# Kernel tuning notes

Hardware: AMD Instinct MI355X
Metric: run time of the kernel (lower is better)

## Reference

```python
import jax, jax.numpy as jnp
import numpy as np

N, E = 50000, 800000
IN_DIM, HID, OUT, HEADS = 128, 128, 64, 4
C1 = HID // HEADS  # 32 per-head channels in gat1
NEG_SLOPE = 0.2


def _gat_conv(x, src, dst, W, a_src, a_dst, b, heads, ch):
    """PyG GATConv (inference): gather -> edge attention -> segment softmax -> scatter."""
    n = x.shape[0]
    h = (x @ W).reshape(n, heads, ch)                      # [N,H,C]
    alpha_src = jnp.einsum('nhc,hc->nh', h, a_src)         # [N,H]
    alpha_dst = jnp.einsum('nhc,hc->nh', h, a_dst)         # [N,H]
    e = jax.nn.leaky_relu(alpha_src[src] + alpha_dst[dst], NEG_SLOPE)  # [E,H]
    m = jax.ops.segment_max(e, dst, num_segments=n)        # per-target max (stable softmax)
    e = jnp.exp(e - m[dst])
    denom = jax.ops.segment_sum(e, dst, num_segments=n)
    alpha = e / (denom[dst] + 1e-16)                       # [E,H]
    out = jax.ops.segment_sum(h[src] * alpha[:, :, None], dst, num_segments=n)  # [N,H,C]
    return out.reshape(n, heads * ch) + b


def setup_inputs() -> dict:
    key = jax.random.key(0)
    ks = jax.random.split(key, 16)
    x = jax.random.normal(ks[0], (N, IN_DIM), dtype=jnp.float32)
    edge_index = jax.random.randint(ks[1], (2, E), 0, N, dtype=jnp.int64)
    s = lambda fan_in: 1.0 / np.sqrt(fan_in)
    return {
        'x': x,
        'edge_index': edge_index,
        'W1': jax.random.normal(ks[2], (IN_DIM, HEADS * C1), jnp.float32) * s(IN_DIM),
        'a_src1': jax.random.normal(ks[3], (HEADS, C1), jnp.float32) * s(C1),
        'a_dst1': jax.random.normal(ks[4], (HEADS, C1), jnp.float32) * s(C1),
        'b1': jnp.zeros((HID,), jnp.float32),
        'W2': jax.random.normal(ks[5], (HID, OUT), jnp.float32) * s(HID),
        'a_src2': jax.random.normal(ks[6], (1, OUT), jnp.float32) * s(OUT),
        'a_dst2': jax.random.normal(ks[7], (1, OUT), jnp.float32) * s(OUT),
        'b2': jnp.zeros((OUT,), jnp.float32),
        'pw1': jax.random.normal(ks[8], (OUT, OUT), jnp.float32) * s(OUT),
        'pb1': jnp.zeros((OUT,), jnp.float32),
        'pw2': jax.random.normal(ks[9], (OUT, OUT), jnp.float32) * s(OUT),
        'pb2': jnp.zeros((OUT,), jnp.float32),
    }


def reference(x, edge_index, W1, a_src1, a_dst1, b1, W2, a_src2, a_dst2, b2, pw1, pb1, pw2, pb2):
    n = x.shape[0]
    # PyG GATConv add_self_loops=True
    loops = jnp.arange(n, dtype=edge_index.dtype)
    src = jnp.concatenate([edge_index[0], loops])
    dst = jnp.concatenate([edge_index[1], loops])
    h = jax.nn.elu(_gat_conv(x, src, dst, W1, a_src1, a_dst1, b1, HEADS, C1))
    h = jax.nn.elu(_gat_conv(h, src, dst, W2, a_src2, a_dst2, b2, 1, OUT))
    # origin_proj: Linear -> ReLU -> Linear
    h = jax.nn.relu(h @ pw1 + pb1)
    return h @ pw2 + pb2
```

## Files before the change

### kernel.cpp

```cpp
#include <hip/hip_runtime.h>
#include <math.h>

#define N_NODES 50000
#define N_EDGES 800000
#define ET (N_EDGES + N_NODES)
#define IN_DIM 128
#define HID 128
#define OUT_DIM 64
#define BW 64
#define NBUCK ((N_NODES + BW - 1) / BW)
#define NBLK 256
#define EPB 3328
#define NT64 ((N_NODES + 63) / 64)

typedef __attribute__((ext_vector_type(8))) short bf16x8;
typedef __attribute__((ext_vector_type(4))) float f32x4;

__device__ __forceinline__ float lrelu(float x){ return x >= 0.f ? x : 0.2f * x; }
__device__ __forceinline__ float eluf(float x){ return x > 0.f ? x : expm1f(x); }
__device__ __forceinline__ unsigned f2bf(float f){
    unsigned u = __float_as_uint(f);
    return (u + 0x7fffu + ((u >> 16) & 1u)) >> 16;
}
__device__ __forceinline__ float bflo(unsigned u){ return __uint_as_float(u << 16); }
__device__ __forceinline__ float bfhi(unsigned u){ return __uint_as_float(u & 0xffff0000u); }

__global__ __launch_bounds__(256) void k_count(const int* __restrict__ dst, int* __restrict__ C)
{
    __shared__ int cnt[NBUCK];
    const int tid = threadIdx.x, blk = blockIdx.x;
    for (int i = tid; i < NBUCK; i += 256) cnt[i] = 0;
    __syncthreads();
    #pragma unroll
    for (int j = 0; j < EPB / 256; j++) {
        const int e = blk * EPB + j * 256 + tid;
        if (e < ET) {
            const int d = (e < N_EDGES) ? dst[e] : (e - N_EDGES);
            atomicAdd(&cnt[d >> 6], 1);
        }
    }
    __syncthreads();
    for (int b = tid; b < NBUCK; b += 256) C[b * NBLK + blk] = cnt[b];
}

__global__ __launch_bounds__(256) void k_bsumA(const int* __restrict__ C, int* __restrict__ bsum2)
{
    __shared__ int red[4];
    int v = C[blockIdx.x * NBLK + threadIdx.x];
    #pragma unroll
    for (int off = 32; off > 0; off >>= 1) v += __shfl_down(v, off);
    if ((threadIdx.x & 63) == 0) red[threadIdx.x >> 6] = v;
    __syncthreads();
    if (threadIdx.x == 0) bsum2[blockIdx.x] = red[0] + red[1] + red[2] + red[3];
}

__global__ __launch_bounds__(1024) void k_bscanB(const int* __restrict__ bsum2, int* __restrict__ boff2)
{
    __shared__ int part[1024];
    const int t = threadIdx.x;
    int v = (t < NBUCK) ? bsum2[t] : 0;
    part[t] = v;
    __syncthreads();
    #pragma unroll
    for (int d = 1; d < 1024; d <<= 1) {
        int add = (t >= d) ? part[t - d] : 0;
        __syncthreads();
        part[t] += add;
        __syncthreads();
    }
    if (t < NBUCK) boff2[t] = part[t] - v;
    if (t == 0) boff2[NBUCK] = ET;
}

__global__ __launch_bounds__(256) void k_cscanC(const int* __restrict__ C,
                                                const int* __restrict__ boff2,
                                                int* __restrict__ Cs)
{
    __shared__ int part[256];
    const int t = threadIdx.x, b = blockIdx.x;
    int v = C[b * NBLK + t];
    part[t] = v;
    __syncthreads();
    #pragma unroll
    for (int d = 1; d < 256; d <<= 1) {
        int add = (t >= d) ? part[t - d] : 0;
        __syncthreads();
        part[t] += add;
        __syncthreads();
    }
    Cs[b * NBLK + t] = boff2[b] + part[t] - v;
}

__global__ __launch_bounds__(256, 2) void k_gemm1_part2(
    const float* __restrict__ x, const float* __restrict__ W1,
    const float* __restrict__ a_s, const float* __restrict__ a_d,
    unsigned* __restrict__ h1b, float* __restrict__ as1, float* __restrict__ ad1,
    const int* __restrict__ src, const int* __restrict__ dst,
    const int* __restrict__ Cs, uint2* __restrict__ part)
{
    __shared__ unsigned smem[128 * 68 + 64 * 68];
    const int tid = threadIdx.x;

    if (blockIdx.x < NT64) {
        unsigned* sWt = smem;
        unsigned* sxb = smem + 128 * 68;
        const int wave = tid >> 6;
        const int lane = tid & 63;
        const int ll   = lane & 15;
        const int quad = lane >> 4;
        const int n0 = blockIdx.x * 64;

        for (int idx = tid; idx < 8192; idx += 256) {
            const int n = idx & 127, kp = idx >> 7;
            const float w0 = W1[(2 * kp) * 128 + n];
            const float w1 = W1[(2 * kp + 1) * 128 + n];
            sWt[n * 68 + kp] = f2bf(w0) | (f2bf(w1) << 16);
        }
        for (int idx = tid; idx < 4096; idx += 256) {
            const int node = idx >> 6, kp = idx & 63;
            const int n = n0 + node;
            unsigned pk = 0;
            if (n < N_NODES) {
                const float x0 = x[n * 128 + 2 * kp];
                const float x1 = x[n * 128 + 2 * kp + 1];
                pk = f2bf(x0) | (f2bf(x1) << 16);
            }
            sxb[node * 68 + kp] = pk;
        }
        __syncthreads();

        f32x4 acc[8];
        #pragma unroll
        for (int t = 0; t < 8; t++) acc[t] = (f32x4){0.f, 0.f, 0.f, 0.f};

        #pragma unroll
        for (int kk = 0; kk < 4; kk++) {
            const int kpo = 16 * kk + 4 * quad;
            const bf16x8 a = *(const bf16x8*)&sxb[(16 * wave + ll) * 68 + kpo];
            #pragma unroll
            for (int t = 0; t < 8; t++) {
                const bf16x8 b = *(const bf16x8*)&sWt[(16 * t + ll) * 68 + kpo];
                acc[t] = __builtin_amdgcn_mfma_f32_16x16x32_bf16(a, b, acc[t], 0, 0, 0);
            }
        }

        float as_v[8], ad_v[8];
        #pragma unroll
        for (int t = 0; t < 8; t++) { as_v[t] = a_s[16 * t + ll]; ad_v[t] = a_d[16 * t + ll]; }
        unsigned short* h1u = (unsigned short*)h1b;
        #pragma unroll
        for (int r = 0; r < 4; r++) {
            const int n = n0 + 16 * wave + 4 * quad + r;
            float ps0 = acc[0][r] * as_v[0] + acc[1][r] * as_v[1];
            float ps1 = acc[2][r] * as_v[2] + acc[3][r] * as_v[3];
            float ps2 = acc[4][r] * as_v[4] + acc[5][r] * as_v[5];
            float ps3 = acc[6][r] * as_v[6] + acc[7][r] * as_v[7];
            float pd0 = acc[0][r] * ad_v[0] + acc[1][r] * ad_v[1];
            float pd1 = acc[2][r] * ad_v[2] + acc[3][r] * ad_v[3];
            float pd2 = acc[4][r] * ad_v[4] + acc[5][r] * ad_v[5];
            float pd3 = acc[6][r] * ad_v[6] + acc[7][r] * ad_v[7];
            #pragma unroll
            for (int off = 1; off < 16; off <<= 1) {
                ps0 += __shfl_xor(ps0, off); ps1 += __shfl_xor(ps1, off);
                ps2 += __shfl_xor(ps2, off); ps3 += __shfl_xor(ps3, off);
                pd0 += __shfl_xor(pd0, off); pd1 += __shfl_xor(pd1, off);
                pd2 += __shfl_xor(pd2, off); pd3 += __shfl_xor(pd3, off);
            }
            if (n < N_NODES) {
                #pragma unroll
                for (int t = 0; t < 8; t++)
                    h1u[n * 128 + 16 * t + ll] = (unsigned short)f2bf(acc[t][r]);
                if (ll == 0) {
                    as1[n * 4 + 0] = ps0; as1[n * 4 + 1] = ps1;
                    as1[n * 4 + 2] = ps2; as1[n * 4 + 3] = ps3;
                    ad1[n * 4 + 0] = pd0; ad1[n * 4 + 1] = pd1;
                    ad1[n * 4 + 2] = pd2; ad1[n * 4 + 3] = pd3;
                }
            }
        }
    } else {
        const int blk = blockIdx.x - NT64;
        int* base = (int*)smem;
        int* cnt  = (int*)smem + NBUCK;
        for (int b = tid; b < NBUCK; b += 256) { base[b] = Cs[b * NBLK + blk]; cnt[b] = 0; }
        __syncthreads();
        #pragma unroll
        for (int j = 0; j < EPB / 256; j++) {
            const int e = blk * EPB + j * 256 + tid;
            if (e < ET) {
                int s, d;
                if (e < N_EDGES) { s = src[e]; d = dst[e]; } else { s = d = e - N_EDGES; }
                const int b = d >> 6;
                const int r = atomicAdd(&cnt[b], 1);
                part[base[b] + r] = make_uint2((unsigned)d, (unsigned)s);
            }
        }
    }
}

__global__ __launch_bounds__(256) void k_scat2(const int* __restrict__ boff2,
                                               const uint2* __restrict__ part,
                                               int* __restrict__ rowptr,
                                               int* __restrict__ csr_src)
{
    __shared__ int cnt64[BW];
    __shared__ int nbase[BW];
    const int b = blockIdx.x, tid = threadIdx.x;
    const int n0 = b * BW;
    const int lo = boff2[b], hi = boff2[b + 1];
    if (tid < BW) cnt64[tid] = 0;
    __syncthreads();
    for (int i = lo + tid; i < hi; i += 256) {
        atomicAdd(&cnt64[part[i].x & (BW - 1)], 1);
    }
    __syncthreads();
    if (tid < BW) {
        int v = cnt64[tid];
        int incl = v;
        #pragma unroll
        for (int off = 1; off < 64; off <<= 1) {
            int t2 = __shfl_up(incl, off);
            if (tid >= off) incl += t2;
        }
        const int excl = incl - v;
        nbase[tid] = excl;
        const int n = n0 + tid;
        if (n < N_NODES) rowptr[n] = lo + excl;
        cnt64[tid] = 0;
    }
    if (b == 0 && tid == 0) rowptr[N_NODES] = ET;
    __syncthreads();
    for (int i = lo + tid; i < hi; i += 256) {
        const uint2 p = part[i];
        const int dn = (int)p.x & (BW - 1);
        const int r = atomicAdd(&cnt64[dn], 1);
        csr_src[lo + nbase[dn] + r] = (int)p.y;
    }
}

__global__ __launch_bounds__(256) void k_aggr1(
    const int* __restrict__ rowptr, const int* __restrict__ csr_src,
    const float* __restrict__ as1, const float* __restrict__ ad1,
    const uint4* __restrict__ h1u4, const float* __restrict__ b1,
    unsigned* __restrict__ hEb)
{
    const int d  = blockIdx.x * 16 + (threadIdx.x >> 4);
    const int c8 = threadIdx.x & 15;
    const int hd = c8 >> 2;
    const int r0 = rowptr[d], r1 = rowptr[d + 1];
    const float adv = ad1[d * 4 + hd];
    float den = 0.f;
    float acc[8];
    #pragma unroll
    for (int m = 0; m < 8; m++) acc[m] = 0.f;
    int i = r0;
    for (; i + 4 <= r1; i += 4) {
        const int s0 = csr_src[i],     s1 = csr_src[i + 1];
        const int s2 = csr_src[i + 2], s3 = csr_src[i + 3];
        const float e0 = as1[s0 * 4 + hd], e1 = as1[s1 * 4 + hd];
        const float e2 = as1[s2 * 4 + hd], e3 = as1[s3 * 4 + hd];
        const uint4 u0 = h1u4[s0 * 16 + c8];
        const uint4 u1 = h1u4[s1 * 16 + c8];
        const uint4 u2 = h1u4[s2 * 16 + c8];
        const uint4 u3 = h1u4[s3 * 16 + c8];
        const float w0 = expf(lrelu(e0 + adv));
        const float w1 = expf(lrelu(e1 + adv));
        const float w2 = expf(lrelu(e2 + adv));
        const float w3 = expf(lrelu(e3 + adv));
        den += (w0 + w1) + (w2 + w3);
        acc[0] = fmaf(bflo(u0.x), w0, acc[0]); acc[1] = fmaf(bfhi(u0.x), w0, acc[1]);
        acc[2] = fmaf(bflo(u0.y), w0, acc[2]); acc[3] = fmaf(bfhi(u0.y), w0, acc[3]);
        acc[4] = fmaf(bflo(u0.z), w0, acc[4]); acc[5] = fmaf(bfhi(u0.z), w0, acc[5]);
        acc[6] = fmaf(bflo(u0.w), w0, acc[6]); acc[7] = fmaf(bfhi(u0.w), w0, acc[7]);
        acc[0] = fmaf(bflo(u1.x), w1, acc[0]); acc[1] = fmaf(bfhi(u1.x), w1, acc[1]);
        acc[2] = fmaf(bflo(u1.y), w1, acc[2]); acc[3] = fmaf(bfhi(u1.y), w1, acc[3]);
        acc[4] = fmaf(bflo(u1.z), w1, acc[4]); acc[5] = fmaf(bfhi(u1.z), w1, acc[5]);
        acc[6] = fmaf(bflo(u1.w), w1, acc[6]); acc[7] = fmaf(bfhi(u1.w), w1, acc[7]);
        acc[0] = fmaf(bflo(u2.x), w2, acc[0]); acc[1] = fmaf(bfhi(u2.x), w2, acc[1]);
        acc[2] = fmaf(bflo(u2.y), w2, acc[2]); acc[3] = fmaf(bfhi(u2.y), w2, acc[3]);
        acc[4] = fmaf(bflo(u2.z), w2, acc[4]); acc[5] = fmaf(bfhi(u2.z), w2, acc[5]);
        acc[6] = fmaf(bflo(u2.w), w2, acc[6]); acc[7] = fmaf(bfhi(u2.w), w2, acc[7]);
        acc[0] = fmaf(bflo(u3.x), w3, acc[0]); acc[1] = fmaf(bfhi(u3.x), w3, acc[1]);
        acc[2] = fmaf(bflo(u3.y), w3, acc[2]); acc[3] = fmaf(bfhi(u3.y), w3, acc[3]);
        acc[4] = fmaf(bflo(u3.z), w3, acc[4]); acc[5] = fmaf(bfhi(u3.z), w3, acc[5]);
        acc[6] = fmaf(bflo(u3.w), w3, acc[6]); acc[7] = fmaf(bfhi(u3.w), w3, acc[7]);
    }
    for (; i < r1; ++i) {
        const int s = csr_src[i];
        const float w = expf(lrelu(as1[s * 4 + hd] + adv));
        const uint4 u = h1u4[s * 16 + c8];
        den += w;
        acc[0] = fmaf(bflo(u.x), w, acc[0]); acc[1] = fmaf(bfhi(u.x), w, acc[1]);
        acc[2] = fmaf(bflo(u.y), w, acc[2]); acc[3] = fmaf(bfhi(u.y), w, acc[3]);
        acc[4] = fmaf(bflo(u.z), w, acc[4]); acc[5] = fmaf(bfhi(u.z), w, acc[5]);
        acc[6] = fmaf(bflo(u.w), w, acc[6]); acc[7] = fmaf(bfhi(u.w), w, acc[7]);
    }
    const float inv = 1.f / (den + 1e-16f);
    const float4 bA = ((const float4*)b1)[2 * c8];
    const float4 bB = ((const float4*)b1)[2 * c8 + 1];
    const float v0 = eluf(acc[0] * inv + bA.x);
    const float v1 = eluf(acc[1] * inv + bA.y);
    const float v2 = eluf(acc[2] * inv + bA.z);
    const float v3 = eluf(acc[3] * inv + bA.w);
    const float v4 = eluf(acc[4] * inv + bB.x);
    const float v5 = eluf(acc[5] * inv + bB.y);
    const float v6 = eluf(acc[6] * inv + bB.z);
    const float v7 = eluf(acc[7] * inv + bB.w);
    uint4 o;
    o.x = f2bf(v0) | (f2bf(v1) << 16);
    o.y = f2bf(v2) | (f2bf(v3) << 16);
    o.z = f2bf(v4) | (f2bf(v5) << 16);
    o.w = f2bf(v6) | (f2bf(v7) << 16);
    ((uint4*)hEb)[d * 16 + c8] = o;
}

__global__ __launch_bounds__(256, 4) void k_layer2(
    const unsigned* __restrict__ hEb,
    const float* __restrict__ W2, const float* __restrict__ a_s2, const float* __restrict__ a_d2,
    unsigned* __restrict__ h2b, float* __restrict__ as2, float* __restrict__ ad2)
{
    __shared__ unsigned sWt[64 * 68];
    __shared__ unsigned sxb[64 * 68];
    const int tid = threadIdx.x;
    const int wave = tid >> 6;
    const int lane = tid & 63;
    const int ll   = lane & 15;
    const int quad = lane >> 4;
    const int n0 = blockIdx.x * 64;

    for (int idx = tid; idx < 4096; idx += 256) {
        const int n = idx & 63, kp = idx >> 6;
        const float w0 = W2[(2 * kp) * 64 + n];
        const float w1 = W2[(2 * kp + 1) * 64 + n];
        sWt[n * 68 + kp] = f2bf(w0) | (f2bf(w1) << 16);
    }
    const uint4* hE4 = (const uint4*)hEb;
    for (int idx = tid; idx < 1024; idx += 256) {
        const int node = idx >> 4, q = idx & 15;
        const int n = n0 + node;
        uint4 pk = make_uint4(0, 0, 0, 0);
        if (n < N_NODES) pk = hE4[n * 16 + q];
        unsigned* dstp = &sxb[node * 68 + 4 * q];
        dstp[0] = pk.x; dstp[1] = pk.y; dstp[2] = pk.z; dstp[3] = pk.w;
    }
    __syncthreads();

    f32x4 acc[4];
    #pragma unroll
    for (int t = 0; t < 4; t++) acc[t] = (f32x4){0.f, 0.f, 0.f, 0.f};

    #pragma unroll
    for (int kk = 0; kk < 4; kk++) {
        const int kpo = 16 * kk + 4 * quad;
        const bf16x8 a = *(const bf16x8*)&sxb[(16 * wave + ll) * 68 + kpo];
        #pragma unroll
        for (int t = 0; t < 4; t++) {
            const bf16x8 b = *(const bf16x8*)&sWt[(16 * t + ll) * 68 + kpo];
            acc[t] = __builtin_amdgcn_mfma_f32_16x16x32_bf16(a, b, acc[t], 0, 0, 0);
        }
    }

    float as_v[4], ad_v[4];
    #pragma unroll
    for (int t = 0; t < 4; t++) { as_v[t] = a_s2[16 * t + ll]; ad_v[t] = a_d2[16 * t + ll]; }
    unsigned short* h2u = (unsigned short*)h2b;
    #pragma unroll
    for (int r = 0; r < 4; r++) {
        const int n = n0 + 16 * wave + 4 * quad + r;
        float ps = acc[0][r] * as_v[0] + acc[1][r] * as_v[1]
                 + acc[2][r] * as_v[2] + acc[3][r] * as_v[3];
        float pd = acc[0][r] * ad_v[0] + acc[1][r] * ad_v[1]
                 + acc[2][r] * ad_v[2] + acc[3][r] * ad_v[3];
        #pragma unroll
        for (int off = 1; off < 16; off <<= 1) {
            ps += __shfl_xor(ps, off);
            pd += __shfl_xor(pd, off);
        }
        if (n < N_NODES) {
            #pragma unroll
            for (int t = 0; t < 4; t++)
                h2u[n * 64 + 16 * t + ll] = (unsigned short)f2bf(acc[t][r]);
            if (ll == 0) { as2[n] = ps; ad2[n] = pd; }
        }
    }
}

__global__ __launch_bounds__(512, 4) void k_tail(
    const int* __restrict__ rowptr, const int* __restrict__ csr_src,
    const float* __restrict__ as2, const float* __restrict__ ad2,
    const uint4* __restrict__ h2u4, const float* __restrict__ b2,
    const float* __restrict__ pw1, const float* __restrict__ pb1,
    const float* __restrict__ pw2, const float* __restrict__ pb2,
    float* __restrict__ out)
{
    __shared__ float s1[64 * 64];
    __shared__ float s2[64 * 64];
    __shared__ float so[64][68];
    __shared__ float sp[64][68];
    const int tid = threadIdx.x;
    const int n0 = blockIdx.x * 64;

    for (int i = tid; i < 1024; i += 512) {
        ((float4*)s1)[i] = ((const float4*)pw1)[i];
        ((float4*)s2)[i] = ((const float4*)pw2)[i];
    }

    {
        const int dl = tid >> 3;
        const int c8 = tid & 7;
        const int d = n0 + dl;
        float acc[8];
        #pragma unroll
        for (int m = 0; m < 8; m++) acc[m] = 0.f;
        float v0 = 0.f, v1 = 0.f, v2 = 0.f, v3 = 0.f;
        float v4 = 0.f, v5 = 0.f, v6 = 0.f, v7 = 0.f;
        if (d < N_NODES) {
            const int r0 = rowptr[d], r1 = rowptr[d + 1];
            const float adv = ad2[d];
            float den = 0.f;
            int i = r0;
            for (; i + 4 <= r1; i += 4) {
                const int s0 = csr_src[i],     s1_ = csr_src[i + 1];
                const int s2_ = csr_src[i + 2], s3_ = csr_src[i + 3];
                const float e0 = as2[s0], e1 = as2[s1_], e2 = as2[s2_], e3 = as2[s3_];
                const uint4 u0 = h2u4[s0  * 8 + c8];
                const uint4 u1 = h2u4[s1_ * 8 + c8];
                const uint4 u2 = h2u4[s2_ * 8 + c8];
                const uint4 u3 = h2u4[s3_ * 8 + c8];
                const float w0 = expf(lrelu(e0 + adv));
                const float w1 = expf(lrelu(e1 + adv));
                const float w2 = expf(lrelu(e2 + adv));
                const float w3 = expf(lrelu(e3 + adv));
                den += (w0 + w1) + (w2 + w3);
                acc[0] = fmaf(bflo(u0.x), w0, acc[0]); acc[1] = fmaf(bfhi(u0.x), w0, acc[1]);
                acc[2] = fmaf(bflo(u0.y), w0, acc[2]); acc[3] = fmaf(bfhi(u0.y), w0, acc[3]);
                acc[4] = fmaf(bflo(u0.z), w0, acc[4]); acc[5] = fmaf(bfhi(u0.z), w0, acc[5]);
                acc[6] = fmaf(bflo(u0.w), w0, acc[6]); acc[7] = fmaf(bfhi(u0.w), w0, acc[7]);
                acc[0] = fmaf(bflo(u1.x), w1, acc[0]); acc[1] = fmaf(bfhi(u1.x), w1, acc[1]);
                acc[2] = fmaf(bflo(u1.y), w1, acc[2]); acc[3] = fmaf(bfhi(u1.y), w1, acc[3]);
                acc[4] = fmaf(bflo(u1.z), w1, acc[4]); acc[5] = fmaf(bfhi(u1.z), w1, acc[5]);
                acc[6] = fmaf(bflo(u1.w), w1, acc[6]); acc[7] = fmaf(bfhi(u1.w), w1, acc[7]);
                acc[0] = fmaf(bflo(u2.x), w2, acc[0]); acc[1] = fmaf(bfhi(u2.x), w2, acc[1]);
                acc[2] = fmaf(bflo(u2.y), w2, acc[2]); acc[3] = fmaf(bfhi(u2.y), w2, acc[3]);
                acc[4] = fmaf(bflo(u2.z), w2, acc[4]); acc[5] = fmaf(bfhi(u2.z), w2, acc[5]);
                acc[6] = fmaf(bflo(u2.w), w2, acc[6]); acc[7] = fmaf(bfhi(u2.w), w2, acc[7]);
                acc[0] = fmaf(bflo(u3.x), w3, acc[0]); acc[1] = fmaf(bfhi(u3.x), w3, acc[1]);
                acc[2] = fmaf(bflo(u3.y), w3, acc[2]); acc[3] = fmaf(bfhi(u3.y), w3, acc[3]);
                acc[4] = fmaf(bflo(u3.z), w3, acc[4]); acc[5] = fmaf(bfhi(u3.z), w3, acc[5]);
                acc[6] = fmaf(bflo(u3.w), w3, acc[6]); acc[7] = fmaf(bfhi(u3.w), w3, acc[7]);
            }
            for (; i < r1; ++i) {
                const int s = csr_src[i];
                const float w = expf(lrelu(as2[s] + adv));
                const uint4 u = h2u4[s * 8 + c8];
                den += w;
                acc[0] = fmaf(bflo(u.x), w, acc[0]); acc[1] = fmaf(bfhi(u.x), w, acc[1]);
                acc[2] = fmaf(bflo(u.y), w, acc[2]); acc[3] = fmaf(bfhi(u.y), w, acc[3]);
                acc[4] = fmaf(bflo(u.z), w, acc[4]); acc[5] = fmaf(bfhi(u.z), w, acc[5]);
                acc[6] = fmaf(bflo(u.w), w, acc[6]); acc[7] = fmaf(bfhi(u.w), w, acc[7]);
            }
            const float inv = 1.f / (den + 1e-16f);
            const float4 bA = ((const float4*)b2)[2 * c8];
            const float4 bB = ((const float4*)b2)[2 * c8 + 1];
            v0 = eluf(acc[0] * inv + bA.x);
            v1 = eluf(acc[1] * inv + bA.y);
            v2 = eluf(acc[2] * inv + bA.z);
            v3 = eluf(acc[3] * inv + bA.w);
            v4 = eluf(acc[4] * inv + bB.x);
            v5 = eluf(acc[5] * inv + bB.y);
            v6 = eluf(acc[6] * inv + bB.z);
            v7 = eluf(acc[7] * inv + bB.w);
        }
        *(float4*)&so[dl][8 * c8]     = make_float4(v0, v1, v2, v3);
        *(float4*)&so[dl][8 * c8 + 4] = make_float4(v4, v5, v6, v7);
    }
    __syncthreads();

    const int cg = tid & 15;
    const int ng = tid >> 4;
    const float4 pb1_4 = ((const float4*)pb1)[cg];
    const float4 pb2_4 = ((const float4*)pb2)[cg];
    float4 p[2];
    #pragma unroll
    for (int m = 0; m < 2; m++) p[m] = pb1_4;
    #pragma unroll 8
    for (int k = 0; k < 64; k++) {
        const float4 w = *(const float4*)&s1[k * 64 + 4 * cg];
        #pragma unroll
        for (int m = 0; m < 2; m++) {
            const float xv = so[2 * ng + m][k];
            p[m].x = fmaf(xv, w.x, p[m].x);
            p[m].y = fmaf(xv, w.y, p[m].y);
            p[m].z = fmaf(xv, w.z, p[m].z);
            p[m].w = fmaf(xv, w.w, p[m].w);
        }
    }
    #pragma unroll
    for (int m = 0; m < 2; m++) {
        p[m].x = fmaxf(p[m].x, 0.f); p[m].y = fmaxf(p[m].y, 0.f);
        p[m].z = fmaxf(p[m].z, 0.f); p[m].w = fmaxf(p[m].w, 0.f);
        *(float4*)&sp[2 * ng + m][4 * cg] = p[m];
    }
    __syncthreads();
    float4 o[2];
    #pragma unroll
    for (int m = 0; m < 2; m++) o[m] = pb2_4;
    #pragma unroll 8
    for (int k = 0; k < 64; k++) {
        const float4 w = *(const float4*)&s2[k * 64 + 4 * cg];
        #pragma unroll
        for (int m = 0; m < 2; m++) {
            const float xv = sp[2 * ng + m][k];
            o[m].x = fmaf(xv, w.x, o[m].x);
            o[m].y = fmaf(xv, w.y, o[m].y);
            o[m].z = fmaf(xv, w.z, o[m].z);
            o[m].w = fmaf(xv, w.w, o[m].w);
        }
    }
    #pragma unroll
    for (int m = 0; m < 2; m++) {
        const int n = n0 + 2 * ng + m;
        if (n < N_NODES) ((float4*)out)[n * 16 + cg] = o[m];
    }
}

extern "C" void kernel_launch(void* const* d_in, const int* in_sizes, int n_in,
                              void* d_out, int out_size, void* d_ws, size_t ws_size,
                              hipStream_t stream)
{
    const float* x      = (const float*)d_in[0];
    const int*   ei     = (const int*)d_in[1];
    const int*   src    = ei;
    const int*   dst    = ei + N_EDGES;
    const float* W1     = (const float*)d_in[2];
    const float* a_src1 = (const float*)d_in[3];
    const float* a_dst1 = (const float*)d_in[4];
    const float* b1     = (const float*)d_in[5];
    const float* W2     = (const float*)d_in[6];
    const float* a_src2 = (const float*)d_in[7];
    const float* a_dst2 = (const float*)d_in[8];
    const float* b2     = (const float*)d_in[9];
    const float* pw1    = (const float*)d_in[10];
    const float* pb1    = (const float*)d_in[11];
    const float* pw2    = (const float*)d_in[12];
    const float* pb2    = (const float*)d_in[13];

    uint2* part  = (uint2*)d_ws;
    int* ibase   = (int*)(part + ET);
    int* rowptr  = ibase;
    int* C       = rowptr + 50001;
    int* Cs      = C + 200192;
    int* bsum2   = Cs + 200192;
    int* boff2   = bsum2 + 782;
    int* csr_src = boff2 + 785;
    unsigned* h1b = (unsigned*)(csr_src + 850000);
    unsigned* h2b = h1b + 3200000;
    float* fws   = (float*)(h2b + 1600000);
    float* as1   = fws;
    float* ad1   = as1 + 200000;
    unsigned* hEb = (unsigned*)(ad1 + 200000);
    float* as2   = (float*)(hEb + 3200000);
    float* ad2   = as2 + 50000;

    k_count<<<NBLK, 256, 0, stream>>>(dst, C);
    k_bsumA<<<NBUCK, 256, 0, stream>>>(C, bsum2);
    k_bscanB<<<1, 1024, 0, stream>>>(bsum2, boff2);
    k_cscanC<<<NBUCK, 256, 0, stream>>>(C, boff2, Cs);

    k_gemm1_part2<<<NT64 + NBLK, 256, 0, stream>>>(x, W1, a_src1, a_dst1,
                                                   h1b, as1, ad1,
                                                   src, dst, Cs, part);
    k_scat2<<<NBUCK, 256, 0, stream>>>(boff2, part, rowptr, csr_src);

    k_aggr1<<<N_NODES / 16, 256, 0, stream>>>(rowptr, csr_src, as1, ad1,
                                              (const uint4*)h1b, b1, hEb);

    k_layer2<<<NT64, 256, 0, stream>>>(hEb, W2, a_src2, a_dst2, h2b, as2, ad2);

    k_tail<<<NT64, 512, 0, stream>>>(rowptr, csr_src, as2, ad2,
                                     (const uint4*)h2b, b2,
                                     pw1, pb1, pw2, pb2, (float*)d_out);
}
```

Measured before the change: 224.1 us.

## Fuse layer-1 aggregation with layer-2 GEMM and fold bucket sums into count

The layer-1 attention aggregation now writes its ELU'd bf16 rows straight into shared memory, and the same block runs the layer-2 MFMA projection. This removes the hEb round trip through global memory and one kernel launch. Per-bucket totals are now accumulated with atomics inside k_count after a memset, which replaces the separate k_bsumA kernel. k_tail reuses one shared buffer for both MLP stages to raise occupancy, at the cost of an extra barrier. Only 128 of 512 threads do the MFMA work, and 8 waves per block wait at the barrier behind the slowest gather.

```diff
diff --git a/kernel.cpp b/kernel.cpp
--- a/kernel.cpp
+++ b/kernel.cpp
@@ -12,6 +12,7 @@
 #define NBLK 256
 #define EPB 3328
 #define NT64 ((N_NODES + 63) / 64)
+#define NT32 ((N_NODES + 31) / 32)
 
 typedef __attribute__((ext_vector_type(8))) short bf16x8;
 typedef __attribute__((ext_vector_type(4))) float f32x4;
@@ -25,7 +26,9 @@
 __device__ __forceinline__ float bflo(unsigned u){ return __uint_as_float(u << 16); }
 __device__ __forceinline__ float bfhi(unsigned u){ return __uint_as_float(u & 0xffff0000u); }
 
-__global__ __launch_bounds__(256) void k_count(const int* __restrict__ dst, int* __restrict__ C)
+__global__ __launch_bounds__(256) void k_count(const int* __restrict__ dst,
+                                               int* __restrict__ C,
+                                               int* __restrict__ bsum2)
 {
     __shared__ int cnt[NBUCK];
     const int tid = threadIdx.x, blk = blockIdx.x;
@@ -40,18 +43,11 @@
         }
     }
     __syncthreads();
-    for (int b = tid; b < NBUCK; b += 256) C[b * NBLK + blk] = cnt[b];
-}
-
-__global__ __launch_bounds__(256) void k_bsumA(const int* __restrict__ C, int* __restrict__ bsum2)
-{
-    __shared__ int red[4];
-    int v = C[blockIdx.x * NBLK + threadIdx.x];
-    #pragma unroll
-    for (int off = 32; off > 0; off >>= 1) v += __shfl_down(v, off);
-    if ((threadIdx.x & 63) == 0) red[threadIdx.x >> 6] = v;
-    __syncthreads();
-    if (threadIdx.x == 0) bsum2[blockIdx.x] = red[0] + red[1] + red[2] + red[3];
+    for (int b = tid; b < NBUCK; b += 256) {
+        const int v = cnt[b];
+        C[b * NBLK + blk] = v;
+        if (v) atomicAdd(&bsum2[b], v);
+    }
 }
 
 __global__ __launch_bounds__(1024) void k_bscanB(const int* __restrict__ bsum2, int* __restrict__ boff2)
@@ -238,154 +234,149 @@
     }
 }
 
-__global__ __launch_bounds__(256) void k_aggr1(
+__global__ __launch_bounds__(512, 8) void k_aggr1_l2(
     const int* __restrict__ rowptr, const int* __restrict__ csr_src,
     const float* __restrict__ as1, const float* __restrict__ ad1,
     const uint4* __restrict__ h1u4, const float* __restrict__ b1,
-    unsigned* __restrict__ hEb)
-{
-    const int d  = blockIdx.x * 16 + (threadIdx.x >> 4);
-    const int c8 = threadIdx.x & 15;
-    const int hd = c8 >> 2;
-    const int r0 = rowptr[d], r1 = rowptr[d + 1];
-    const float adv = ad1[d * 4 + hd];
-    float den = 0.f;
-    float acc[8];
-    #pragma unroll
-    for (int m = 0; m < 8; m++) acc[m] = 0.f;
-    int i = r0;
-    for (; i + 4 <= r1; i += 4) {
-        const int s0 = csr_src[i],     s1 = csr_src[i + 1];
-        const int s2 = csr_src[i + 2], s3 = csr_src[i + 3];
-        const float e0 = as1[s0 * 4 + hd], e1 = as1[s1 * 4 + hd];
-        const float e2 = as1[s2 * 4 + hd], e3 = as1[s3 * 4 + hd];
-        const uint4 u0 = h1u4[s0 * 16 + c8];
-        const uint4 u1 = h1u4[s1 * 16 + c8];
-        const uint4 u2 = h1u4[s2 * 16 + c8];
-        const uint4 u3 = h1u4[s3 * 16 + c8];
-        const float w0 = expf(lrelu(e0 + adv));
-        const float w1 = expf(lrelu(e1 + adv));
-        const float w2 = expf(lrelu(e2 + adv));
-        const float w3 = expf(lrelu(e3 + adv));
-        den += (w0 + w1) + (w2 + w3);
-        acc[0] = fmaf(bflo(u0.x), w0, acc[0]); acc[1] = fmaf(bfhi(u0.x), w0, acc[1]);
-        acc[2] = fmaf(bflo(u0.y), w0, acc[2]); acc[3] = fmaf(bfhi(u0.y), w0, acc[3]);
-        acc[4] = fmaf(bflo(u0.z), w0, acc[4]); acc[5] = fmaf(bfhi(u0.z), w0, acc[5]);
-        acc[6] = fmaf(bflo(u0.w), w0, acc[6]); acc[7] = fmaf(bfhi(u0.w), w0, acc[7]);
-        acc[0] = fmaf(bflo(u1.x), w1, acc[0]); acc[1] = fmaf(bfhi(u1.x), w1, acc[1]);
-        acc[2] = fmaf(bflo(u1.y), w1, acc[2]); acc[3] = fmaf(bfhi(u1.y), w1, acc[3]);
-        acc[4] = fmaf(bflo(u1.z), w1, acc[4]); acc[5] = fmaf(bfhi(u1.z), w1, acc[5]);
-        acc[6] = fmaf(bflo(u1.w), w1, acc[6]); acc[7] = fmaf(bfhi(u1.w), w1, acc[7]);
-        acc[0] = fmaf(bflo(u2.x), w2, acc[0]); acc[1] = fmaf(bfhi(u2.x), w2, acc[1]);
-        acc[2] = fmaf(bflo(u2.y), w2, acc[2]); acc[3] = fmaf(bfhi(u2.y), w2, acc[3]);
-        acc[4] = fmaf(bflo(u2.z), w2, acc[4]); acc[5] = fmaf(bfhi(u2.z), w2, acc[5]);
-        acc[6] = fmaf(bflo(u2.w), w2, acc[6]); acc[7] = fmaf(bfhi(u2.w), w2, acc[7]);
-        acc[0] = fmaf(bflo(u3.x), w3, acc[0]); acc[1] = fmaf(bfhi(u3.x), w3, acc[1]);
-        acc[2] = fmaf(bflo(u3.y), w3, acc[2]); acc[3] = fmaf(bfhi(u3.y), w3, acc[3]);
-        acc[4] = fmaf(bflo(u3.z), w3, acc[4]); acc[5] = fmaf(bfhi(u3.z), w3, acc[5]);
-        acc[6] = fmaf(bflo(u3.w), w3, acc[6]); acc[7] = fmaf(bfhi(u3.w), w3, acc[7]);
-    }
-    for (; i < r1; ++i) {
-        const int s = csr_src[i];
-        const float w = expf(lrelu(as1[s * 4 + hd] + adv));
-        const uint4 u = h1u4[s * 16 + c8];
-        den += w;
-        acc[0] = fmaf(bflo(u.x), w, acc[0]); acc[1] = fmaf(bfhi(u.x), w, acc[1]);
-        acc[2] = fmaf(bflo(u.y), w, acc[2]); acc[3] = fmaf(bfhi(u.y), w, acc[3]);
-        acc[4] = fmaf(bflo(u.z), w, acc[4]); acc[5] = fmaf(bfhi(u.z), w, acc[5]);
-        acc[6] = fmaf(bflo(u.w), w, acc[6]); acc[7] = fmaf(bfhi(u.w), w, acc[7]);
-    }
-    const float inv = 1.f / (den + 1e-16f);
-    const float4 bA = ((const float4*)b1)[2 * c8];
-    const float4 bB = ((const float4*)b1)[2 * c8 + 1];
-    const float v0 = eluf(acc[0] * inv + bA.x);
-    const float v1 = eluf(acc[1] * inv + bA.y);
-    const float v2 = eluf(acc[2] * inv + bA.z);
-    const float v3 = eluf(acc[3] * inv + bA.w);
-    const float v4 = eluf(acc[4] * inv + bB.x);
-    const float v5 = eluf(acc[5] * inv + bB.y);
-    const float v6 = eluf(acc[6] * inv + bB.z);
-    const float v7 = eluf(acc[7] * inv + bB.w);
-    uint4 o;
-    o.x = f2bf(v0) | (f2bf(v1) << 16);
-    o.y = f2bf(v2) | (f2bf(v3) << 16);
-    o.z = f2bf(v4) | (f2bf(v5) << 16);
-    o.w = f2bf(v6) | (f2bf(v7) << 16);
-    ((uint4*)hEb)[d * 16 + c8] = o;
-}
-
-__global__ __launch_bounds__(256, 4) void k_layer2(
-    const unsigned* __restrict__ hEb,
     const float* __restrict__ W2, const float* __restrict__ a_s2, const float* __restrict__ a_d2,
     unsigned* __restrict__ h2b, float* __restrict__ as2, float* __restrict__ ad2)
 {
     __shared__ unsigned sWt[64 * 68];
-    __shared__ unsigned sxb[64 * 68];
+    __shared__ unsigned sxb[32 * 68];
     const int tid = threadIdx.x;
-    const int wave = tid >> 6;
-    const int lane = tid & 63;
-    const int ll   = lane & 15;
-    const int quad = lane >> 4;
-    const int n0 = blockIdx.x * 64;
-
-    for (int idx = tid; idx < 4096; idx += 256) {
+    const int n0 = blockIdx.x * 32;
+
+    for (int idx = tid; idx < 4096; idx += 512) {
         const int n = idx & 63, kp = idx >> 6;
         const float w0 = W2[(2 * kp) * 64 + n];
         const float w1 = W2[(2 * kp + 1) * 64 + n];
         sWt[n * 68 + kp] = f2bf(w0) | (f2bf(w1) << 16);
     }
-    const uint4* hE4 = (const uint4*)hEb;
-    for (int idx = tid; idx < 1024; idx += 256) {
-        const int node = idx >> 4, q = idx & 15;
-        const int n = n0 + node;
-        uint4 pk = make_uint4(0, 0, 0, 0);
-        if (n < N_NODES) pk = hE4[n * 16 + q];
-        unsigned* dstp = &sxb[node * 68 + 4 * q];
-        dstp[0] = pk.x; dstp[1] = pk.y; dstp[2] = pk.z; dstp[3] = pk.w;
-    }
-    __syncthreads();
-
-    f32x4 acc[4];
-    #pragma unroll
-    for (int t = 0; t < 4; t++) acc[t] = (f32x4){0.f, 0.f, 0.f, 0.f};
-
-    #pragma unroll
-    for (int kk = 0; kk < 4; kk++) {
-        const int kpo = 16 * kk + 4 * quad;
-        const bf16x8 a = *(const bf16x8*)&sxb[(16 * wave + ll) * 68 + kpo];
-        #pragma unroll
-        for (int t = 0; t < 4; t++) {
-            const bf16x8 b = *(const bf16x8*)&sWt[(16 * t + ll) * 68 + kpo];
-            acc[t] = __builtin_amdgcn_mfma_f32_16x16x32_bf16(a, b, acc[t], 0, 0, 0);
-        }
-    }
-
-    float as_v[4], ad_v[4];
-    #pragma unroll
-    for (int t = 0; t < 4; t++) { as_v[t] = a_s2[16 * t + ll]; ad_v[t] = a_d2[16 * t + ll]; }
-    unsigned short* h2u = (unsigned short*)h2b;
-    #pragma unroll
-    for (int r = 0; r < 4; r++) {
-        const int n = n0 + 16 * wave + 4 * quad + r;
-        float ps = acc[0][r] * as_v[0] + acc[1][r] * as_v[1]
-                 + acc[2][r] * as_v[2] + acc[3][r] * as_v[3];
-        float pd = acc[0][r] * ad_v[0] + acc[1][r] * ad_v[1]
-                 + acc[2][r] * ad_v[2] + acc[3][r] * ad_v[3];
-        #pragma unroll
-        for (int off = 1; off < 16; off <<= 1) {
-            ps += __shfl_xor(ps, off);
-            pd += __shfl_xor(pd, off);
-        }
-        if (n < N_NODES) {
+
+    {
+        const int dl = tid >> 4;
+        const int c8 = tid & 15;
+        const int hd = c8 >> 2;
+        const int d = n0 + dl;
+        uint4 o = make_uint4(0, 0, 0, 0);
+        if (d < N_NODES) {
+            const int r0 = rowptr[d], r1 = rowptr[d + 1];
+            const float adv = ad1[d * 4 + hd];
+            float den = 0.f;
+            float acc[8];
             #pragma unroll
-            for (int t = 0; t < 4; t++)
-                h2u[n * 64 + 16 * t + ll] = (unsigned short)f2bf(acc[t][r]);
-            if (ll == 0) { as2[n] = ps; ad2[n] = pd; }
-        }
-    }
-}
-
-__global__ __launch_bounds__(512, 4) void k_tail(
+            for (int m = 0; m < 8; m++) acc[m] = 0.f;
+            int i = r0;
+            for (; i + 4 <= r1; i += 4) {
+                const int s0 = csr_src[i],     s1 = csr_src[i + 1];
+                const int s2 = csr_src[i + 2], s3 = csr_src[i + 3];
+                const float e0 = as1[s0 * 4 + hd], e1 = as1[s1 * 4 + hd];
+                const float e2 = as1[s2 * 4 + hd], e3 = as1[s3 * 4 + hd];
+                const uint4 u0 = h1u4[s0 * 16 + c8];
+                const uint4 u1 = h1u4[s1 * 16 + c8];
+                const uint4 u2 = h1u4[s2 * 16 + c8];
+                const uint4 u3 = h1u4[s3 * 16 + c8];
+                const float w0 = expf(lrelu(e0 + adv));
+                const float w1 = expf(lrelu(e1 + adv));
+                const float w2 = expf(lrelu(e2 + adv));
+                const float w3 = expf(lrelu(e3 + adv));
+                den += (w0 + w1) + (w2 + w3);
+                acc[0] = fmaf(bflo(u0.x), w0, acc[0]); acc[1] = fmaf(bfhi(u0.x), w0, acc[1]);
+                acc[2] = fmaf(bflo(u0.y), w0, acc[2]); acc[3] = fmaf(bfhi(u0.y), w0, acc[3]);
+                acc[4] = fmaf(bflo(u0.z), w0, acc[4]); acc[5] = fmaf(bfhi(u0.z), w0, acc[5]);
+                acc[6] = fmaf(bflo(u0.w), w0, acc[6]); acc[7] = fmaf(bfhi(u0.w), w0, acc[7]);
+                acc[0] = fmaf(bflo(u1.x), w1, acc[0]); acc[1] = fmaf(bfhi(u1.x), w1, acc[1]);
+                acc[2] = fmaf(bflo(u1.y), w1, acc[2]); acc[3] = fmaf(bfhi(u1.y), w1, acc[3]);
+                acc[4] = fmaf(bflo(u1.z), w1, acc[4]); acc[5] = fmaf(bfhi(u1.z), w1, acc[5]);
+                acc[6] = fmaf(bflo(u1.w), w1, acc[6]); acc[7] = fmaf(bfhi(u1.w), w1, acc[7]);
+                acc[0] = fmaf(bflo(u2.x), w2, acc[0]); acc[1] = fmaf(bfhi(u2.x), w2, acc[1]);
+                acc[2] = fmaf(bflo(u2.y), w2, acc[2]); acc[3] = fmaf(bfhi(u2.y), w2, acc[3]);
+                acc[4] = fmaf(bflo(u2.z), w2, acc[4]); acc[5] = fmaf(bfhi(u2.z), w2, acc[5]);
+                acc[6] = fmaf(bflo(u2.w), w2, acc[6]); acc[7] = fmaf(bfhi(u2.w), w2, acc[7]);
+                acc[0] = fmaf(bflo(u3.x), w3, acc[0]); acc[1] = fmaf(bfhi(u3.x), w3, acc[1]);
+                acc[2] = fmaf(bflo(u3.y), w3, acc[2]); acc[3] = fmaf(bfhi(u3.y), w3, acc[3]);
+                acc[4] = fmaf(bflo(u3.z), w3, acc[4]); acc[5] = fmaf(bfhi(u3.z), w3, acc[5]);
+                acc[6] = fmaf(bflo(u3.w), w3, acc[6]); acc[7] = fmaf(bfhi(u3.w), w3, acc[7]);
+            }
+            for (; i < r1; ++i) {
+                const int s = csr_src[i];
+                const float w = expf(lrelu(as1[s * 4 + hd] + adv));
+                const uint4 u = h1u4[s * 16 + c8];
+                den += w;
+                acc[0] = fmaf(bflo(u.x), w, acc[0]); acc[1] = fmaf(bfhi(u.x), w, acc[1]);
+                acc[2] = fmaf(bflo(u.y), w, acc[2]); acc[3] = fmaf(bfhi(u.y), w, acc[3]);
+                acc[4] = fmaf(bflo(u.z), w, acc[4]); acc[5] = fmaf(bfhi(u.z), w, acc[5]);
+                acc[6] = fmaf(bflo(u.w), w, acc[6]); acc[7] = fmaf(bfhi(u.w), w, acc[7]);
+            }
+            const float inv = 1.f / (den + 1e-16f);
+            const float4 bA = ((const float4*)b1)[2 * c8];
+            const float4 bB = ((const float4*)b1)[2 * c8 + 1];
+            const float v0 = eluf(acc[0] * inv + bA.x);
+            const float v1 = eluf(acc[1] * inv + bA.y);
+            const float v2 = eluf(acc[2] * inv + bA.z);
+            const float v3 = eluf(acc[3] * inv + bA.w);
+            const float v4 = eluf(acc[4] * inv + bB.x);
+            const float v5 = eluf(acc[5] * inv + bB.y);
+            const float v6 = eluf(acc[6] * inv + bB.z);
+            const float v7 = eluf(acc[7] * inv + bB.w);
+            o.x = f2bf(v0) | (f2bf(v1) << 16);
+            o.y = f2bf(v2) | (f2bf(v3) << 16);
+            o.z = f2bf(v4) | (f2bf(v5) << 16);
+            o.w = f2bf(v6) | (f2bf(v7) << 16);
+        }
+        unsigned* dstp = &sxb[dl * 68 + 4 * c8];
+        dstp[0] = o.x; dstp[1] = o.y; dstp[2] = o.z; dstp[3] = o.w;
+    }
+    __syncthreads();
+
+    if (tid < 128) {
+        const int wave = tid >> 6;
+        const int lane = tid & 63;
+        const int ll   = lane & 15;
+        const int quad = lane >> 4;
+
+        f32x4 acc[4];
+        #pragma unroll
+        for (int t = 0; t < 4; t++) acc[t] = (f32x4){0.f, 0.f, 0.f, 0.f};
+
+        #pragma unroll
+        for (int kk = 0; kk < 4; kk++) {
+            const int kpo = 16 * kk + 4 * quad;
+            const bf16x8 a = *(const bf16x8*)&sxb[(16 * wave + ll) * 68 + kpo];
+            #pragma unroll
+            for (int t = 0; t < 4; t++) {
+                const bf16x8 b = *(const bf16x8*)&sWt[(16 * t + ll) * 68 + kpo];
+                acc[t] = __builtin_amdgcn_mfma_f32_16x16x32_bf16(a, b, acc[t], 0, 0, 0);
+            }
+        }
+
+        float as_v[4], ad_v[4];
+        #pragma unroll
+        for (int t = 0; t < 4; t++) { as_v[t] = a_s2[16 * t + ll]; ad_v[t] = a_d2[16 * t + ll]; }
+        unsigned short* h2u = (unsigned short*)h2b;
+        #pragma unroll
+        for (int r = 0; r < 4; r++) {
+            const int n = n0 + 16 * wave + 4 * quad + r;
+            float ps = acc[0][r] * as_v[0] + acc[1][r] * as_v[1]
+                     + acc[2][r] * as_v[2] + acc[3][r] * as_v[3];
+            float pd = acc[0][r] * ad_v[0] + acc[1][r] * ad_v[1]
+                     + acc[2][r] * ad_v[2] + acc[3][r] * ad_v[3];
+            #pragma unroll
+            for (int off = 1; off < 16; off <<= 1) {
+                ps += __shfl_xor(ps, off);
+                pd += __shfl_xor(pd, off);
+            }
+            if (n < N_NODES) {
+                #pragma unroll
+                for (int t = 0; t < 4; t++)
+                    h2u[n * 64 + 16 * t + ll] = (unsigned short)f2bf(acc[t][r]);
+                if (ll == 0) { as2[n] = ps; ad2[n] = pd; }
+            }
+        }
+    }
+}
+
+__global__ __launch_bounds__(512, 6) void k_tail(
     const int* __restrict__ rowptr, const int* __restrict__ csr_src,
     const float* __restrict__ as2, const float* __restrict__ ad2,
     const uint4* __restrict__ h2u4, const float* __restrict__ b2,
@@ -393,16 +384,15 @@
     const float* __restrict__ pw2, const float* __restrict__ pb2,
     float* __restrict__ out)
 {
-    __shared__ float s1[64 * 64];
-    __shared__ float s2[64 * 64];
-    __shared__ float so[64][68];
-    __shared__ float sp[64][68];
+    __shared__ float sW1[64 * 64];
+    __shared__ float sW2[64 * 64];
+    __shared__ float sosp[64][68];
     const int tid = threadIdx.x;
     const int n0 = blockIdx.x * 64;
 
     for (int i = tid; i < 1024; i += 512) {
-        ((float4*)s1)[i] = ((const float4*)pw1)[i];
-        ((float4*)s2)[i] = ((const float4*)pw2)[i];
+        ((float4*)sW1)[i] = ((const float4*)pw1)[i];
+        ((float4*)sW2)[i] = ((const float4*)pw2)[i];
     }
 
     {
@@ -420,7 +410,7 @@
             float den = 0.f;
             int i = r0;
             for (; i + 4 <= r1; i += 4) {
-                const int s0 = csr_src[i],     s1_ = csr_src[i + 1];
+                const int s0 = csr_src[i],      s1_ = csr_src[i + 1];
                 const int s2_ = csr_src[i + 2], s3_ = csr_src[i + 3];
                 const float e0 = as2[s0], e1 = as2[s1_], e2 = as2[s2_], e3 = as2[s3_];
                 const uint4 u0 = h2u4[s0  * 8 + c8];
@@ -471,8 +461,8 @@
             v6 = eluf(acc[6] * inv + bB.z);
             v7 = eluf(acc[7] * inv + bB.w);
         }
-        *(float4*)&so[dl][8 * c8]     = make_float4(v0, v1, v2, v3);
-        *(float4*)&so[dl][8 * c8 + 4] = make_float4(v4, v5, v6, v7);
+        *(float4*)&sosp[dl][8 * c8]     = make_float4(v0, v1, v2, v3);
+        *(float4*)&sosp[dl][8 * c8 + 4] = make_float4(v4, v5, v6, v7);
     }
     __syncthreads();
 
@@ -485,32 +475,35 @@
     for (int m = 0; m < 2; m++) p[m] = pb1_4;
     #pragma unroll 8
     for (int k = 0; k < 64; k++) {
-        const float4 w = *(const float4*)&s1[k * 64 + 4 * cg];
+        const float4 w = *(const float4*)&sW1[k * 64 + 4 * cg];
         #pragma unroll
         for (int m = 0; m < 2; m++) {
-            const float xv = so[2 * ng + m][k];
+            const float xv = sosp[2 * ng + m][k];
             p[m].x = fmaf(xv, w.x, p[m].x);
             p[m].y = fmaf(xv, w.y, p[m].y);
             p[m].z = fmaf(xv, w.z, p[m].z);
             p[m].w = fmaf(xv, w.w, p[m].w);
         }
     }
+    __syncthreads();
+
     #pragma unroll
     for (int m = 0; m < 2; m++) {
         p[m].x = fmaxf(p[m].x, 0.f); p[m].y = fmaxf(p[m].y, 0.f);
         p[m].z = fmaxf(p[m].z, 0.f); p[m].w = fmaxf(p[m].w, 0.f);
-        *(float4*)&sp[2 * ng + m][4 * cg] = p[m];
-    }
-    __syncthreads();
+        *(float4*)&sosp[2 * ng + m][4 * cg] = p[m];
+    }
+    __syncthreads();
+
     float4 o[2];
     #pragma unroll
     for (int m = 0; m < 2; m++) o[m] = pb2_4;
     #pragma unroll 8
     for (int k = 0; k < 64; k++) {
-        const float4 w = *(const float4*)&s2[k * 64 + 4 * cg];
+        const float4 w = *(const float4*)&sW2[k * 64 + 4 * cg];
         #pragma unroll
         for (int m = 0; m < 2; m++) {
-            const float xv = sp[2 * ng + m][k];
+            const float xv = sosp[2 * ng + m][k];
             o[m].x = fmaf(xv, w.x, o[m].x);
             o[m].y = fmaf(xv, w.y, o[m].y);
             o[m].z = fmaf(xv, w.z, o[m].z);
@@ -548,22 +541,21 @@
     uint2* part  = (uint2*)d_ws;
     int* ibase   = (int*)(part + ET);
     int* rowptr  = ibase;
-    int* C       = rowptr + 50001;
+    int* C       = rowptr + 50004;
     int* Cs      = C + 200192;
     int* bsum2   = Cs + 200192;
-    int* boff2   = bsum2 + 782;
-    int* csr_src = boff2 + 785;
+    int* boff2   = bsum2 + 784;
+    int* csr_src = boff2 + 784;
     unsigned* h1b = (unsigned*)(csr_src + 850000);
     unsigned* h2b = h1b + 3200000;
     float* fws   = (float*)(h2b + 1600000);
     float* as1   = fws;
     float* ad1   = as1 + 200000;
-    unsigned* hEb = (unsigned*)(ad1 + 200000);
-    float* as2   = (float*)(hEb + 3200000);
+    float* as2   = ad1 + 200000;
     float* ad2   = as2 + 50000;
 
-    k_count<<<NBLK, 256, 0, stream>>>(dst, C);
-    k_bsumA<<<NBUCK, 256, 0, stream>>>(C, bsum2);
+    hipMemsetAsync(bsum2, 0, NBUCK * sizeof(int), stream);
+    k_count<<<NBLK, 256, 0, stream>>>(dst, C, bsum2);
     k_bscanB<<<1, 1024, 0, stream>>>(bsum2, boff2);
     k_cscanC<<<NBUCK, 256, 0, stream>>>(C, boff2, Cs);
 
@@ -572,10 +564,9 @@
                                                    src, dst, Cs, part);
     k_scat2<<<NBUCK, 256, 0, stream>>>(boff2, part, rowptr, csr_src);
 
-    k_aggr1<<<N_NODES / 16, 256, 0, stream>>>(rowptr, csr_src, as1, ad1,
-                                              (const uint4*)h1b, b1, hEb);
-
-    k_layer2<<<NT64, 256, 0, stream>>>(hEb, W2, a_src2, a_dst2, h2b, as2, ad2);
+    k_aggr1_l2<<<NT32, 512, 0, stream>>>(rowptr, csr_src, as1, ad1,
+                                         (const uint4*)h1b, b1,
+                                         W2, a_src2, a_dst2, h2b, as2, ad2);
 
     k_tail<<<NT64, 512, 0, stream>>>(rowptr, csr_src, as2, ad2,
                                      (const uint4*)h2b, b2,
```

Result: slower. 245.9 us (+9.7%).
